# Kernel tuning notes

Hardware: AMD Instinct MI355X
Metric: run time of the kernel (lower is better)

Reference implementation:

```python
import jax, jax.numpy as jnp
import numpy as np

B, C, O, H, W = 8, 64, 64, 128, 128


def conv3x3(x, w, b):
    # x: [B,Cin,H,W], w: [Cout,Cin,3,3], stride 1, padding 1
    y = jax.lax.conv_general_dilated(
        x, w, window_strides=(1, 1), padding=((1, 1), (1, 1)),
        dimension_numbers=("NCHW", "OIHW", "NCHW"))
    return y + b[None, :, None, None]


def setup_inputs() -> dict:
    key = jax.random.key(0)
    ks = jax.random.split(key, 6)
    fan = C * 9
    x = jax.random.normal(ks[0], (B, C, H, W), dtype=jnp.float32)
    w_main = jax.random.normal(ks[1], (O, C, 3, 3), dtype=jnp.float32) / np.sqrt(fan)
    # small offset weights keep sampled locations near the regular grid (realistic post-training regime)
    w_offset = jax.random.normal(ks[2], (18, C, 3, 3), dtype=jnp.float32) * 0.05 / np.sqrt(fan)
    b_offset = jnp.zeros((18,), dtype=jnp.float32)
    w_mask = jax.random.normal(ks[3], (9, C, 3, 3), dtype=jnp.float32) / np.sqrt(fan)
    b_mask = jnp.zeros((9,), dtype=jnp.float32)
    return {"x": x, "w_main": w_main, "w_offset": w_offset,
            "b_offset": b_offset, "w_mask": w_mask, "b_mask": b_mask}


def deform_conv2d(x, w_main, offset, mask):
    # torchvision.ops.deform_conv2d: kernel 3x3, stride 1, pad 1, dilation 1, no bias
    Bb, Cc, Hh, Ww = x.shape
    Oo = w_main.shape[0]
    off = offset.reshape(Bb, 9, 2, Hh, Ww)
    dy, dx = off[:, :, 0], off[:, :, 1]            # [B,9,H,W]; pairs ordered (y,x), k row-major
    k = jnp.arange(9)
    kh = (k // 3 - 1).astype(x.dtype)              # kernel row offset in {-1,0,1}
    kw = (k % 3 - 1).astype(x.dtype)
    iy = jnp.arange(Hh, dtype=x.dtype)
    ix = jnp.arange(Ww, dtype=x.dtype)
    # sampling positions p = p0 + p_k + delta_p
    py = dy + iy[None, None, :, None] + kh[None, :, None, None]
    px = dx + ix[None, None, None, :] + kw[None, :, None, None]

    y0 = jnp.floor(py)
    x0 = jnp.floor(px)
    ly = py - y0
    lx = px - x0
    y0i = y0.astype(jnp.int32)
    x0i = x0.astype(jnp.int32)
    y1i = y0i + 1
    x1i = x0i + 1

    bidx = jnp.arange(Bb)[:, None, None, None]

    def corner(yi, xi, wgt):
        # zero-padding semantics: out-of-bounds neighbors contribute 0
        valid = (yi >= 0) & (yi < Hh) & (xi >= 0) & (xi < Ww)
        v = x[bidx, :, jnp.clip(yi, 0, Hh - 1), jnp.clip(xi, 0, Ww - 1)]  # [B,9,H,W,C]
        return v * (wgt * valid)[..., None]

    samp = (corner(y0i, x0i, (1 - ly) * (1 - lx))
            + corner(y0i, x1i, (1 - ly) * lx)
            + corner(y1i, x0i, ly * (1 - lx))
            + corner(y1i, x1i, ly * lx))
    samp = samp * mask[..., None]                  # modulation mask (dcn v2)
    # contract sampled patches with weights: [B,9,H,W,C] x [O,C,9] -> [B,O,H,W]
    return jnp.einsum("bkhwc,ock->bohw", samp, w_main.reshape(Oo, Cc, 9))


def reference(x, w_main, w_offset, b_offset, w_mask, b_mask):
    offset = conv3x3(x, w_offset, b_offset)                 # [B,18,H,W]
    mask = jax.nn.sigmoid(conv3x3(x, w_mask, b_mask))       # [B,9,H,W]
    return deform_conv2d(x, w_main, offset, mask)
```

## Files before the change

kernel.cpp:

```cpp
#include <hip/hip_runtime.h>
#include <math.h>

#define BB 8
#define CC 64
#define OO 64
#define HH 128
#define WW 128
#define HW (HH*WW)
#define NPIX (BB*HW)

typedef __bf16 bf16x8 __attribute__((ext_vector_type(8)));
typedef float floatx4 __attribute__((ext_vector_type(4)));
typedef float f32x2 __attribute__((ext_vector_type(2)));
typedef unsigned short ushort_t;

#define XT_BYTES  16777216
#define OM_BYTES  14680064
#define WT_BYTES  73728

__device__ __forceinline__ unsigned short f2b(float f) {
    unsigned u = __float_as_uint(f);
    u += 0x7fffu + ((u >> 16) & 1u);
    return (unsigned short)(u >> 16);
}

__device__ __forceinline__ unsigned cvt_pk_bf16(float lo, float hi) {
    unsigned r;
    asm("v_cvt_pk_bf16_f32 %0, %1, %2" : "=v"(r) : "v"(lo), "v"(hi));
    return r;
}

__device__ __forceinline__ f32x2 pk_fma(f32x2 a, f32x2 b, f32x2 c) {
    f32x2 d;
    asm("v_pk_fma_f32 %0, %1, %2, %3" : "=v"(d) : "v"(a), "v"(b), "v"(c));
    return d;
}

__device__ __forceinline__ f32x2 pk_mul(f32x2 a, f32x2 b) {
    f32x2 d;
    asm("v_pk_mul_f32 %0, %1, %2" : "=v"(d) : "v"(a), "v"(b));
    return d;
}

__global__ __launch_bounds__(256) void prep_kernel(
    const float* __restrict__ x,
    const float* __restrict__ wm, const float* __restrict__ woff,
    const float* __restrict__ wmask,
    ushort_t* __restrict__ xt, ushort_t* __restrict__ wt,
    ushort_t* __restrict__ wb)
{
    __shared__ float tile[64][33];
    int bid = blockIdx.x;
    int t   = threadIdx.x;

    if (bid < 4096) {
        int bh = bid >> 2;
        int w0 = (bid & 3) * 32;
        int b  = bh >> 7;
        int h  = bh & 127;

        {
            int c  = t >> 2;
            int wq = t & 3;
            const float* src = x + (((size_t)(b*CC + c))*HH + h)*WW + (w0 + wq*8);
            float4 v0 = ((const float4*)src)[0];
            float4 v1 = ((const float4*)src)[1];
            int wbse = wq*8;
            tile[c][wbse+0] = v0.x; tile[c][wbse+1] = v0.y;
            tile[c][wbse+2] = v0.z; tile[c][wbse+3] = v0.w;
            tile[c][wbse+4] = v1.x; tile[c][wbse+5] = v1.y;
            tile[c][wbse+6] = v1.z; tile[c][wbse+7] = v1.w;
        }
        __syncthreads();
        {
            int w   = t & 31;
            int cg8 = t >> 5;
            unsigned uu[4];
            #pragma unroll
            for (int j = 0; j < 4; ++j)
                uu[j] = cvt_pk_bf16(tile[cg8*8 + 2*j][w], tile[cg8*8 + 2*j + 1][w]);
            *(uint4*)(xt + (((size_t)(b*HH + h))*WW + (w0 + w))*CC + cg8*8)
                = make_uint4(uu[0], uu[1], uu[2], uu[3]);
        }
    } else {
        int i = (bid - 4096) * 256 + t;
        if (i < 36864) {
            int o = i / 576, k = i % 576, tap = k >> 6, c = k & 63;
            wt[i] = f2b(wm[o*576 + c*9 + tap]);
        }
        int j = i - 36864;
        if (j >= 0 && j < 18432) {
            int o = j / 576, k = j % 576, tap = k >> 6, c = k & 63;
            float v = 0.f;
            if (o < 18)      v = woff[o*576 + c*9 + tap];
            else if (o < 27) v = wmask[(o-18)*576 + c*9 + tap];
            wb[j] = f2b(v);
        }
    }
}

__global__ __launch_bounds__(256) void conv27_kernel(
    const ushort_t* __restrict__ xt, const ushort_t* __restrict__ wb,
    const float* __restrict__ boff, const float* __restrict__ bmsk,
    float* __restrict__ om)
{
    __shared__ ushort_t win[18*18*72];
    int bid = blockIdx.x;
    int b  = bid >> 6;
    int th = (bid >> 3) & 7;
    int tw = bid & 7;
    int h0 = th * 16, w0 = tw * 16;
    int t = threadIdx.x;

    for (int idx = t; idx < 18*18*8; idx += 256) {
        int r   = idx / 144;
        int rem = idx - r*144;
        int col = rem >> 3;
        int ch  = (rem & 7) << 3;
        int y = h0 + r - 1, x = w0 + col - 1;
        uint4 val = make_uint4(0,0,0,0);
        if ((unsigned)y < (unsigned)HH && (unsigned)x < (unsigned)WW)
            val = *(const uint4*)(xt + ((((size_t)b*HH + y)*WW + x) << 6) + ch);
        *(uint4*)(win + (r*18 + col)*72 + ch) = val;
    }
    __syncthreads();

    int lane = t & 63, wv = t >> 6;
    int n = lane & 15, quad = lane >> 4;
    const ushort_t* wb0 = wb + n*576;
    const ushort_t* wb1 = wb + (16 + n)*576;

    floatx4 acc0[4], acc1[4];
    #pragma unroll
    for (int mt = 0; mt < 4; ++mt) {
        acc0[mt] = (floatx4){0.f,0.f,0.f,0.f};
        acc1[mt] = (floatx4){0.f,0.f,0.f,0.f};
    }

    #pragma unroll
    for (int s = 0; s < 18; ++s) {
        int tap  = s >> 1;
        int tr   = tap / 3, tc = tap % 3;
        int coff = (s & 1)*32 + quad*8;
        int kk = tap*64 + coff;
        bf16x8 b0 = *(const bf16x8*)(wb0 + kk);
        bf16x8 b1 = *(const bf16x8*)(wb1 + kk);
        #pragma unroll
        for (int mt = 0; mt < 4; ++mt) {
            int ty = wv*4 + mt;
            bf16x8 a = *(const bf16x8*)(win + ((ty + tr)*18 + (n + tc))*72 + coff);
            acc0[mt] = __builtin_amdgcn_mfma_f32_16x16x32_bf16(a, b0, acc0[mt], 0, 0, 0);
            acc1[mt] = __builtin_amdgcn_mfma_f32_16x16x32_bf16(a, b1, acc1[mt], 0, 0, 0);
        }
    }

    #pragma unroll
    for (int mt = 0; mt < 4; ++mt) {
        int ty = wv*4 + mt;
        #pragma unroll
        for (int r = 0; r < 4; ++r) {
            int tx = quad*4 + r;
            size_t p = ((size_t)(b*HH + h0 + ty))*WW + (w0 + tx);
            float* dst = om + p*28;
            dst[n] = acc0[mt][r] + boff[n];
            int o1 = 16 + n;
            if (o1 < 18) {
                dst[o1] = acc1[mt][r] + boff[o1];
            } else if (o1 < 27) {
                float z = acc1[mt][r] + bmsk[o1 - 18];
                dst[o1] = 1.f / (1.f + expf(-z));
            } else if (o1 == 27) {
                dst[27] = 0.f;
            }
        }
    }
}

__device__ __forceinline__ void issue_tap(
    uint4* q, float* cw,
    const ushort_t* xbase, int cg, int h_a, int w_a,
    int kr, int kc, float dy, float dx, float m)
{
    float py = (float)(h_a + kr - 1) + dy;
    float px = (float)(w_a + kc - 1) + dx;
    float y0f = floorf(py), x0f = floorf(px);
    float ly = py - y0f, lx = px - x0f;
    int y0 = (int)y0f, x0 = (int)x0f, y1 = y0 + 1, x1 = x0 + 1;
    float vy0 = ((unsigned)y0 < (unsigned)HH) ? 1.f : 0.f;
    float vy1 = ((unsigned)y1 < (unsigned)HH) ? 1.f : 0.f;
    float vx0 = ((unsigned)x0 < (unsigned)WW) ? 1.f : 0.f;
    float vx1 = ((unsigned)x1 < (unsigned)WW) ? 1.f : 0.f;
    cw[0] = (1.f-ly)*(1.f-lx)*vy0*vx0*m;
    cw[1] = (1.f-ly)*lx      *vy0*vx1*m;
    cw[2] = ly*(1.f-lx)      *vy1*vx0*m;
    cw[3] = ly*lx            *vy1*vx1*m;
    int ys[4] = { y0, y0, y1, y1 };
    int xs[4] = { x0, x1, x0, x1 };
    #pragma unroll
    for (int cn = 0; cn < 4; ++cn) {
        int yc = min(max(ys[cn], 0), HH-1);
        int xc = min(max(xs[cn], 0), WW-1);
        const uint4* cp = (const uint4*)(xbase + (((yc << 7) + xc) << 6) + cg*16);
        q[2*cn]   = cp[0];
        q[2*cn+1] = cp[1];
    }
}

__device__ __forceinline__ void pack_tap(
    const uint4* q, const float* cw, ushort_t* dst)
{
    f32x2 v2[8];
    {
        f32x2 w2; w2.x = cw[0]; w2.y = cw[0];
        unsigned u0[8] = { q[0].x, q[0].y, q[0].z, q[0].w,
                           q[1].x, q[1].y, q[1].z, q[1].w };
        #pragma unroll
        for (int j = 0; j < 8; ++j) {
            f32x2 f;
            f.x = __uint_as_float(u0[j] << 16);
            f.y = __uint_as_float(u0[j] & 0xffff0000u);
            v2[j] = pk_mul(f, w2);
        }
    }
    #pragma unroll
    for (int cn = 1; cn < 4; ++cn) {
        f32x2 w2; w2.x = cw[cn]; w2.y = cw[cn];
        unsigned u0[8] = { q[2*cn].x,   q[2*cn].y,   q[2*cn].z,   q[2*cn].w,
                           q[2*cn+1].x, q[2*cn+1].y, q[2*cn+1].z, q[2*cn+1].w };
        #pragma unroll
        for (int j = 0; j < 8; ++j) {
            f32x2 f;
            f.x = __uint_as_float(u0[j] << 16);
            f.y = __uint_as_float(u0[j] & 0xffff0000u);
            v2[j] = pk_fma(f, w2, v2[j]);
        }
    }
    unsigned uu[8];
    #pragma unroll
    for (int j = 0; j < 8; ++j)
        uu[j] = cvt_pk_bf16(v2[j].x, v2[j].y);
    uint4* d = (uint4*)dst;
    d[0] = make_uint4(uu[0], uu[1], uu[2], uu[3]);
    d[1] = make_uint4(uu[4], uu[5], uu[6], uu[7]);
}

#define SROW 200

__global__ __launch_bounds__(256, 3) void deform_kernel(
    const ushort_t* __restrict__ xt, const float* __restrict__ om,
    const ushort_t* __restrict__ wt, float* __restrict__ out)
{
    __shared__ ushort_t samp[64*SROW];

    int t = threadIdx.x;
    int lane = t & 63, wv = t >> 6;
    int bid = blockIdx.x;
    int b  = bid >> 8;
    int th = (bid >> 4) & 15;
    int tw = bid & 15;
    int h0 = th * 8, w0 = tw * 8;

    int pa = t >> 2, cg = t & 3;
    int ph = pa >> 3, pw = pa & 7;
    int h_a = h0 + ph, w_a = w0 + pw;
    const float* omp = om + (((size_t)(b*HH + h_a))*WW + w_a) * 28;
    const ushort_t* xbase = xt + ((size_t)b << 20);

    int n = lane & 15, quad = lane >> 4;
    floatx4 acc[4];
    #pragma unroll
    for (int i = 0; i < 4; ++i) acc[i] = (floatx4){0.f,0.f,0.f,0.f};
    const ushort_t* wrow = wt + (wv*16 + n)*576 + quad*8;

    uint4 q[2][8];
    float cw[2][4];

    float dyv[3], dxv[3], mv[3];
    #pragma unroll
    for (int j = 0; j < 3; ++j) {
        dyv[j] = omp[2*j]; dxv[j] = omp[2*j+1]; mv[j] = omp[18+j];
    }
    issue_tap(q[0], cw[0], xbase, cg, h_a, w_a, 0, 0, dyv[0], dxv[0], mv[0]);

    #pragma unroll
    for (int p = 0; p < 3; ++p) {
        bf16x8 wf[6];
        #pragma unroll
        for (int s = 0; s < 6; ++s)
            wf[s] = *(const bf16x8*)(wrow + (p*6 + s)*32);

        float dyn_[3], dxn_[3], mn_[3];
        if (p < 2) {
            #pragma unroll
            for (int j = 0; j < 3; ++j) {
                int k2 = 3*(p+1) + j;
                dyn_[j] = omp[2*k2]; dxn_[j] = omp[2*k2+1]; mn_[j] = omp[18+k2];
            }
        }

        #pragma unroll
        for (int kk = 0; kk < 3; ++kk) {
            int g = 3*p + kk;
            if (g < 8) {
                if (kk < 2)
                    issue_tap(q[(g+1)&1], cw[(g+1)&1], xbase, cg, h_a, w_a,
                              p, kk+1, dyv[kk+1], dxv[kk+1], mv[kk+1]);
                else
                    issue_tap(q[(g+1)&1], cw[(g+1)&1], xbase, cg, h_a, w_a,
                              p+1, 0, dyn_[0], dxn_[0], mn_[0]);
            }
            pack_tap(q[g&1], cw[g&1], samp + pa*SROW + kk*64 + cg*16);
        }

        __syncthreads();

        __builtin_amdgcn_s_setprio(1);
        #pragma unroll
        for (int kk = 0; kk < 3; ++kk) {
            #pragma unroll
            for (int half = 0; half < 2; ++half) {
                bf16x8 bfrag = wf[kk*2 + half];
                #pragma unroll
                for (int mt = 0; mt < 4; ++mt) {
                    bf16x8 afrag = *(const bf16x8*)(samp + (mt*16 + n)*SROW
                                                    + kk*64 + half*32 + quad*8);
                    acc[mt] = __builtin_amdgcn_mfma_f32_16x16x32_bf16(
                                  afrag, bfrag, acc[mt], 0, 0, 0);
                }
            }
        }
        __builtin_amdgcn_s_setprio(0);

        if (p < 2) {
            __syncthreads();
            #pragma unroll
            for (int j = 0; j < 3; ++j) {
                dyv[j] = dyn_[j]; dxv[j] = dxn_[j]; mv[j] = mn_[j];
            }
        }
    }

    float* op = out + ((size_t)b*OO + (wv*16 + n))*HW;
    #pragma unroll
    for (int mt = 0; mt < 4; ++mt) {
        int row = h0 + mt*2 + (quad >> 1);
        int col = w0 + (quad & 1)*4;
        float4 st = make_float4(acc[mt][0], acc[mt][1], acc[mt][2], acc[mt][3]);
        *(float4*)(op + row*WW + col) = st;
    }
}

extern "C" void kernel_launch(void* const* d_in, const int* in_sizes, int n_in,
                              void* d_out, int out_size, void* d_ws, size_t ws_size,
                              hipStream_t stream)
{
    const float* x      = (const float*)d_in[0];
    const float* w_main = (const float*)d_in[1];
    const float* w_off  = (const float*)d_in[2];
    const float* b_off  = (const float*)d_in[3];
    const float* w_msk  = (const float*)d_in[4];
    const float* b_msk  = (const float*)d_in[5];
    float* out = (float*)d_out;

    unsigned char* ws = (unsigned char*)d_ws;
    ushort_t* xt = (ushort_t*)ws;
    float*    om = (float*)(ws + XT_BYTES);
    ushort_t* wt = (ushort_t*)(ws + XT_BYTES + OM_BYTES);
    ushort_t* wb = (ushort_t*)(ws + XT_BYTES + OM_BYTES + WT_BYTES);

    prep_kernel<<<4096 + 216, 256, 0, stream>>>(x, w_main, w_off, w_msk, xt, wt, wb);

    conv27_kernel<<<NPIX/256, 256, 0, stream>>>(xt, wb, b_off, b_msk, om);

    deform_kernel<<<NPIX/64, 256, 0, stream>>>(xt, om, wt, out);
}
```

Before: 158.0 us.

## Shrink deform tile to 32 pixels with two waves each covering 32 outputs

The deform kernel now uses 128-thread blocks, each handling a 4x8 pixel tile instead of 8x8, and twice as many blocks are launched. Each wave now computes 32 output channels using two weight fragment sets, reusing each A fragment across two MFMAs. This halves the shared-memory tile and should raise occupancy and block count, giving better latency hiding for the gathers. In exchange, each block does half the MFMA work per barrier, there are more blocks, and weight fragment registers double.

```diff
diff --git a/kernel.cpp b/kernel.cpp
--- a/kernel.cpp
+++ b/kernel.cpp
@@ -246,31 +246,34 @@
 
 #define SROW 200
 
-__global__ __launch_bounds__(256, 3) void deform_kernel(
+__global__ __launch_bounds__(128, 3) void deform_kernel(
     const ushort_t* __restrict__ xt, const float* __restrict__ om,
     const ushort_t* __restrict__ wt, float* __restrict__ out)
 {
-    __shared__ ushort_t samp[64*SROW];
+    __shared__ ushort_t samp[32*SROW];
 
     int t = threadIdx.x;
     int lane = t & 63, wv = t >> 6;
     int bid = blockIdx.x;
-    int b  = bid >> 8;
-    int th = (bid >> 4) & 15;
+    int b  = bid >> 9;
+    int th = (bid >> 4) & 31;
     int tw = bid & 15;
-    int h0 = th * 8, w0 = tw * 8;
+    int h0 = th * 4, w0 = tw * 8;
 
     int pa = t >> 2, cg = t & 3;
-    int ph = pa >> 3, pw = pa & 7;
-    int h_a = h0 + ph, w_a = w0 + pw;
+    int h_a = h0 + (pa >> 3), w_a = w0 + (pa & 7);
     const float* omp = om + (((size_t)(b*HH + h_a))*WW + w_a) * 28;
     const ushort_t* xbase = xt + ((size_t)b << 20);
 
     int n = lane & 15, quad = lane >> 4;
-    floatx4 acc[4];
-    #pragma unroll
-    for (int i = 0; i < 4; ++i) acc[i] = (floatx4){0.f,0.f,0.f,0.f};
-    const ushort_t* wrow = wt + (wv*16 + n)*576 + quad*8;
+    floatx4 acc[2][2];
+    #pragma unroll
+    for (int i = 0; i < 2; ++i)
+        #pragma unroll
+        for (int j = 0; j < 2; ++j)
+            acc[i][j] = (floatx4){0.f,0.f,0.f,0.f};
+    const ushort_t* wrow0 = wt + (wv*32 + n)*576 + quad*8;
+    const ushort_t* wrow1 = wt + (wv*32 + 16 + n)*576 + quad*8;
 
     uint4 q[2][8];
     float cw[2][4];
@@ -284,10 +287,12 @@
 
     #pragma unroll
     for (int p = 0; p < 3; ++p) {
-        bf16x8 wf[6];
-        #pragma unroll
-        for (int s = 0; s < 6; ++s)
-            wf[s] = *(const bf16x8*)(wrow + (p*6 + s)*32);
+        bf16x8 wf0[6], wf1[6];
+        #pragma unroll
+        for (int s = 0; s < 6; ++s) {
+            wf0[s] = *(const bf16x8*)(wrow0 + (p*6 + s)*32);
+            wf1[s] = *(const bf16x8*)(wrow1 + (p*6 + s)*32);
+        }
 
         float dyn_[3], dxn_[3], mn_[3];
         if (p < 2) {
@@ -319,13 +324,14 @@
         for (int kk = 0; kk < 3; ++kk) {
             #pragma unroll
             for (int half = 0; half < 2; ++half) {
-                bf16x8 bfrag = wf[kk*2 + half];
                 #pragma unroll
-                for (int mt = 0; mt < 4; ++mt) {
+                for (int mt = 0; mt < 2; ++mt) {
                     bf16x8 afrag = *(const bf16x8*)(samp + (mt*16 + n)*SROW
                                                     + kk*64 + half*32 + quad*8);
-                    acc[mt] = __builtin_amdgcn_mfma_f32_16x16x32_bf16(
-                                  afrag, bfrag, acc[mt], 0, 0, 0);
+                    acc[0][mt] = __builtin_amdgcn_mfma_f32_16x16x32_bf16(
+                                     afrag, wf0[kk*2 + half], acc[0][mt], 0, 0, 0);
+                    acc[1][mt] = __builtin_amdgcn_mfma_f32_16x16x32_bf16(
+                                     afrag, wf1[kk*2 + half], acc[1][mt], 0, 0, 0);
                 }
             }
         }
@@ -340,13 +346,17 @@
         }
     }
 
-    float* op = out + ((size_t)b*OO + (wv*16 + n))*HW;
-    #pragma unroll
-    for (int mt = 0; mt < 4; ++mt) {
-        int row = h0 + mt*2 + (quad >> 1);
-        int col = w0 + (quad & 1)*4;
-        float4 st = make_float4(acc[mt][0], acc[mt][1], acc[mt][2], acc[mt][3]);
-        *(float4*)(op + row*WW + col) = st;
+    #pragma unroll
+    for (int og = 0; og < 2; ++og) {
+        float* op = out + ((size_t)b*OO + (wv*32 + og*16 + n))*HW;
+        #pragma unroll
+        for (int mt = 0; mt < 2; ++mt) {
+            int row = h0 + mt*2 + (quad >> 1);
+            int col = w0 + (quad & 1)*4;
+            float4 st = make_float4(acc[og][mt][0], acc[og][mt][1],
+                                    acc[og][mt][2], acc[og][mt][3]);
+            *(float4*)(op + row*WW + col) = st;
+        }
     }
 }
 
@@ -372,5 +382,5 @@
 
     conv27_kernel<<<NPIX/256, 256, 0, stream>>>(xt, wb, b_off, b_msk, om);
 
-    deform_kernel<<<NPIX/64, 256, 0, stream>>>(xt, om, wt, out);
-}
+    deform_kernel<<<NPIX/32, 128, 0, stream>>>(xt, om, wt, out);
+}
```

After: 173.4 us. 1.1x slower.
